# Performance work log

Hardware: AMD Instinct MI355X
Metric: run time of the kernel (lower is better)

## Reference

```python
import jax, jax.numpy as jnp
import numpy as np

N_ITERS = 2
N_NODES = 50000
N_EDGES = 400000
NODE_DIM = 128
EDGE_DIM = 128
MLP_HIDDEN = 128


def _gru_cell(x, h, W_ih, W_hh, b_ih, b_hh):
    # torch.nn.GRUCell math. W_ih: [3H, in], W_hh: [3H, H]
    gi = x @ W_ih.T + b_ih
    gh = h @ W_hh.T + b_hh
    i_r, i_z, i_n = jnp.split(gi, 3, axis=-1)
    h_r, h_z, h_n = jnp.split(gh, 3, axis=-1)
    r = jax.nn.sigmoid(i_r + h_r)
    z = jax.nn.sigmoid(i_z + h_z)
    n = jnp.tanh(i_n + r * h_n)
    return (1.0 - z) * n + z * h


def _edge_softmax(logits, dst, num_nodes):
    # logits: [E], normalized over incoming edges of each dst node
    m = jax.ops.segment_max(logits, dst, num_segments=num_nodes)
    e = jnp.exp(logits - m[dst])
    s = jax.ops.segment_sum(e, dst, num_segments=num_nodes)
    return e / s[dst]


def setup_inputs() -> dict:
    key = jax.random.key(0)
    ks = jax.random.split(key, 20)
    s = 0.05
    inp = {
        'nf': jax.random.normal(ks[0], (N_NODES, NODE_DIM), jnp.float32),
        'ef': jax.random.normal(ks[1], (N_EDGES, EDGE_DIM), jnp.float32),
        'src': jax.random.randint(ks[2], (N_EDGES,), 0, N_NODES, jnp.int32),
        'dst': jax.random.randint(ks[3], (N_EDGES,), 0, N_NODES, jnp.int32),
        # edge GRUCell: input 2*node_dim -> hidden edge_dim
        'eW_ih': s * jax.random.normal(ks[4], (3 * EDGE_DIM, 2 * NODE_DIM), jnp.float32),
        'eW_hh': s * jax.random.normal(ks[5], (3 * EDGE_DIM, EDGE_DIM), jnp.float32),
        'eb_ih': s * jax.random.normal(ks[6], (3 * EDGE_DIM,), jnp.float32),
        'eb_hh': s * jax.random.normal(ks[7], (3 * EDGE_DIM,), jnp.float32),
        # node GRUCell: input edge_dim -> hidden node_dim
        'nW_ih': s * jax.random.normal(ks[8], (3 * NODE_DIM, EDGE_DIM), jnp.float32),
        'nW_hh': s * jax.random.normal(ks[9], (3 * NODE_DIM, NODE_DIM), jnp.float32),
        'nb_ih': s * jax.random.normal(ks[10], (3 * NODE_DIM,), jnp.float32),
        'nb_hh': s * jax.random.normal(ks[11], (3 * NODE_DIM,), jnp.float32),
        # attention MLP: edge_dim -> hidden -> 1
        'aW1': s * jax.random.normal(ks[12], (EDGE_DIM, MLP_HIDDEN), jnp.float32),
        'ab1': jnp.zeros((MLP_HIDDEN,), jnp.float32),
        'aW2': s * jax.random.normal(ks[13], (MLP_HIDDEN, 1), jnp.float32),
        'ab2': jnp.zeros((1,), jnp.float32),
    }
    return inp


def reference(nf, ef, src, dst, eW_ih, eW_hh, eb_ih, eb_hh,
              nW_ih, nW_hh, nb_ih, nb_hh, aW1, ab1, aW2, ab2):
    num_nodes = nf.shape[0]
    for _ in range(N_ITERS):
        # per-edge GRU update: input = [src_h ; dst_h], hidden = edge feature
        x_e = jnp.concatenate([nf[src], nf[dst]], axis=-1)  # [E, 2*node_dim]
        uef = _gru_cell(x_e, ef, eW_ih, eW_hh, eb_ih, eb_hh)  # [E, edge_dim]
        # attention MLP + edge softmax over destination neighborhoods
        logits = (jax.nn.relu(uef @ aW1 + ab1) @ aW2 + ab2)[:, 0]  # [E]
        attn = _edge_softmax(logits, dst, num_nodes)  # [E]
        # weighted scatter-sum aggregation to destination nodes
        agg_m = jax.ops.segment_sum(uef * attn[:, None], dst, num_segments=num_nodes)
        # node GRU update
        unf = _gru_cell(agg_m, nf, nW_ih, nW_hh, nb_ih, nb_hh)  # [N, node_dim]
        nf, ef = unf, uef
    return (nf, ef)
```

## Files before the change

kernel.cpp:

```cpp
#include <hip/hip_runtime.h>

#define NN 50000
#define NE 400000
#define DIM 128

typedef __bf16 bf16x8 __attribute__((ext_vector_type(8)));
typedef float f32x4 __attribute__((ext_vector_type(4)));
typedef unsigned short u16;

#define MFMA16 __builtin_amdgcn_mfma_f32_16x16x32_bf16

__device__ __forceinline__ u16 f2b(float f){ __bf16 b=(__bf16)f; return __builtin_bit_cast(u16,b); }
__device__ __forceinline__ float b2f(u16 h){ unsigned u = ((unsigned)h)<<16; return __builtin_bit_cast(float,u); }
__device__ __forceinline__ float sigm(float x){ return 1.0f/(1.0f+__expf(-x)); }
__device__ __forceinline__ float tanh_(float x){ float e=__expf(2.0f*x); return 1.0f-2.0f/(e+1.0f); }
__device__ __forceinline__ bf16x8 ldb8(const u16* p){ return *reinterpret_cast<const bf16x8*>(p); }

#define GLOAD_LDS(gp, lp) __builtin_amdgcn_global_load_lds( \
    (const __attribute__((address_space(1))) void*)(gp),    \
    (__attribute__((address_space(3))) void*)(lp), 16, 0, 0)

__global__ void f2b_kernel(const float* __restrict__ in, u16* __restrict__ out, int n4){
  int i = blockIdx.x*blockDim.x + threadIdx.x;
  int st = gridDim.x*blockDim.x;
  for (; i<n4; i+=st){
    float4 v = reinterpret_cast<const float4*>(in)[i];
    ushort4 o = { f2b(v.x), f2b(v.y), f2b(v.z), f2b(v.w) };
    reinterpret_cast<ushort4*>(out)[i] = o;
  }
}

__global__ void transpose128_kernel(const float* __restrict__ in, u16* __restrict__ out){
  int i = blockIdx.x*blockDim.x + threadIdx.x;
  int k = i>>7, n = i&127;
  out[n*128+k] = f2b(in[i]);
}

__global__ void zero_kernel(int* p, int n){
  int i = blockIdx.x*blockDim.x + threadIdx.x; if (i<n) p[i]=0;
}
__global__ void hist_kernel(const int* __restrict__ dst, int* __restrict__ counts, int n){
  int i = blockIdx.x*blockDim.x + threadIdx.x; if (i<n) atomicAdd(&counts[dst[i]],1);
}
__global__ void scanA_kernel(const int* __restrict__ counts, int* __restrict__ rowp,
                             int* __restrict__ bsum, int n){
  __shared__ int buf[1024];
  const int gid = blockIdx.x*1024 + threadIdx.x;
  int v = (gid<n) ? counts[gid] : 0;
  buf[threadIdx.x]=v; __syncthreads();
  for (int off=1; off<1024; off<<=1){
    int x = (threadIdx.x>=off) ? buf[threadIdx.x-off] : 0;
    __syncthreads();
    buf[threadIdx.x]+=x; __syncthreads();
  }
  if (gid<n) rowp[gid] = buf[threadIdx.x]-v;
  if (threadIdx.x==1023) bsum[blockIdx.x]=buf[1023];
}
__global__ void scanB_kernel(int* bsum, int* rowp, int nb, int n){
  if (threadIdx.x==0 && blockIdx.x==0){
    int run=0;
    for (int b=0;b<nb;++b){ int t=bsum[b]; bsum[b]=run; run+=t; }
    rowp[n]=run;
  }
}
__global__ void scanC_kernel(int* __restrict__ rowp, int* __restrict__ cursor,
                             const int* __restrict__ bsum, int n){
  const int gid = blockIdx.x*1024 + threadIdx.x;
  if (gid<n){ int v = rowp[gid]+bsum[blockIdx.x]; rowp[gid]=v; cursor[gid]=v; }
}
__global__ void scatter_kernel(const int* __restrict__ dst, int* __restrict__ cursor,
                               int* __restrict__ eids, int n){
  int i = blockIdx.x*blockDim.x + threadIdx.x;
  if (i<n){ int p = atomicAdd(&cursor[dst[i]],1); eids[p]=i; }
}
__global__ void perm_kernel(const int* __restrict__ eids, const int* __restrict__ src,
                            const int* __restrict__ dst, int* __restrict__ srcp,
                            int* __restrict__ dstp, int n){
  int i = blockIdx.x*blockDim.x + threadIdx.x;
  if (i<n){ int e=eids[i]; srcp[i]=src[e]; dstp[i]=dst[e]; }
}
__global__ void efgather_kernel(const int* __restrict__ eids, const float* __restrict__ ef,
                                u16* __restrict__ efb){
  long i = (long)blockIdx.x*256 + threadIdx.x;
  long pos = i>>5; int k4 = (int)(i&31);
  long e = eids[pos];
  float4 v = reinterpret_cast<const float4*>(ef + e*DIM)[k4];
  ushort4 o = { f2b(v.x), f2b(v.y), f2b(v.z), f2b(v.w) };
  reinterpret_cast<ushort4*>(efb + pos*DIM)[k4] = o;
}

__global__ __launch_bounds__(512, 4)
void edge_kernel(const int* __restrict__ srcp, const int* __restrict__ dstp,
                 const int* __restrict__ eids,
                 const u16* __restrict__ nfb, u16* __restrict__ efb,
                 const u16* __restrict__ Wih, const u16* __restrict__ Whh,
                 const float* __restrict__ bih, const float* __restrict__ bhh,
                 const u16* __restrict__ aW1T, const float* __restrict__ ab1,
                 const float* __restrict__ aW2, const float* __restrict__ ab2,
                 float* __restrict__ logits, float* __restrict__ ef32out)
{
  __shared__ __align__(16) u16 wbuf[36*512];
  const int wave = threadIdx.x>>6, lane = threadIdx.x&63;
  const int r16 = lane&15, kq = lane>>4;
  const long base = (long)blockIdx.x*128 + wave*16;
  const long e = base + r16;

  auto stage = [&](int c){
    if (c < 8){
      for (int f = wave; f < 36; f += 8){
        const u16* g;
        if (f < 24){ const int gt = f>>3, s = f&7;
          g = Wih + (long)(gt*128 + c*16 + r16)*256 + s*32 + kq*8; }
        else { const int q = f-24, gt = q>>2, s = q&3;
          g = Whh + (long)(gt*128 + c*16 + r16)*128 + s*32 + kq*8; }
        GLOAD_LDS(g, wbuf + f*512);
      }
    } else {
      for (int f = wave; f < 32; f += 8){
        const int t = f>>2, s = f&3;
        GLOAD_LDS(aW1T + (long)(t*16 + r16)*128 + s*32 + kq*8, wbuf + f*512);
      }
    }
  };

  const u16* sp = nfb + (long)srcp[e]*DIM;
  const u16* dp = nfb + (long)dstp[e]*DIM;
  const u16* ep = efb + e*DIM;
  bf16x8 ag[8], ae[4];
#pragma unroll
  for (int s=0;s<4;++s){
    ag[s]   = ldb8(sp + s*32 + kq*8);
    ag[s+4] = ldb8(dp + s*32 + kq*8);
    ae[s]   = ldb8(ep + s*32 + kq*8);
  }
  int oe[4];
#pragma unroll
  for (int r=0;r<4;++r) oe[r] = eids[base + kq*4 + r];

  stage(0);
  __syncthreads();

  u16* ebase = efb + (base + kq*4)*DIM + r16;
  const float* bi0 = bih + r16;
  const float* bh0 = bhh + r16;

  const f32x4 vzero = {0.f,0.f,0.f,0.f};
  const u16* lbase = wbuf + lane*8;

#pragma unroll 1
  for (int c=0;c<8;++c){
    const int c16 = c*16;
    const float bir=bi0[c16], biz=bi0[c16+DIM], bin=bi0[c16+2*DIM];
    const float bhr=bh0[c16], bhz=bh0[c16+DIM], bhn=bh0[c16+2*DIM];
    float h0p[4];
#pragma unroll
    for (int r=0;r<4;++r) h0p[r] = b2f(ebase[r*DIM + c16]);

    f32x4 ar=vzero, az=vzero, an=vzero, hr=vzero, hz=vzero, hn=vzero;
#pragma unroll
    for (int s=0;s<8;++s){
      ar = MFMA16(ag[s], ldb8(lbase + ( s   )*512), ar,0,0,0);
      az = MFMA16(ag[s], ldb8(lbase + ( 8+s )*512), az,0,0,0);
      an = MFMA16(ag[s], ldb8(lbase + (16+s )*512), an,0,0,0);
    }
#pragma unroll
    for (int s=0;s<4;++s){
      hr = MFMA16(ae[s], ldb8(lbase + (24+s)*512), hr,0,0,0);
      hz = MFMA16(ae[s], ldb8(lbase + (28+s)*512), hz,0,0,0);
      hn = MFMA16(ae[s], ldb8(lbase + (32+s)*512), hn,0,0,0);
    }
    __syncthreads();
    stage(c+1);
    float uv[4];
#pragma unroll
    for (int r=0;r<4;++r){
      float rg = sigm(ar[r]+bir + hr[r]+bhr);
      float zg = sigm(az[r]+biz + hz[r]+bhz);
      float ng = tanh_(an[r]+bin + rg*(hn[r]+bhn));
      float u  = ng + zg*(h0p[r]-ng);
      ebase[r*DIM + c16] = f2b(u);
      uv[r] = u;
    }
    if (ef32out){
#pragma unroll
      for (int r=0;r<4;++r) ef32out[(long)oe[r]*DIM + c16 + r16] = uv[r];
    }
    __syncthreads();
  }

  bf16x8 ua[4];
#pragma unroll
  for (int s=0;s<4;++s) ua[s] = ldb8(ep + s*32 + kq*8);
  float part[4] = {0.f,0.f,0.f,0.f};
#pragma unroll 1
  for (int t=0;t<8;++t){
    f32x4 h = vzero;
#pragma unroll
    for (int s=0;s<4;++s)
      h = MFMA16(ua[s], ldb8(lbase + (t*4+s)*512), h,0,0,0);
    const int cc = t*16 + r16;
    const float b1 = ab1[cc], w2 = aW2[cc];
#pragma unroll
    for (int r=0;r<4;++r) part[r] += fmaxf(h[r]+b1, 0.f)*w2;
  }
#pragma unroll
  for (int off=1; off<16; off<<=1){
#pragma unroll
    for (int r=0;r<4;++r) part[r] += __shfl_xor(part[r], off, 64);
  }
  if (r16==0){
    const float b2v = ab2[0];
#pragma unroll
    for (int r=0;r<4;++r) logits[base + kq*4 + r] = part[r] + b2v;
  }
}

__global__ __launch_bounds__(256)
void agg_kernel(const int* __restrict__ rowp, const float* __restrict__ logits,
                const u16* __restrict__ uefb, u16* __restrict__ aggb)
{
  const int wave = threadIdx.x>>6, lane = threadIdx.x&63;
  const int v = blockIdx.x*4 + wave;
  if (v>=NN) return;
  const int p0 = rowp[v], p1 = rowp[v+1], deg = p1-p0;
  float ax=0.f, ay=0.f;
  if (deg>0){
    float mx = -__builtin_inff();
    for (int i=p0+lane; i<p1; i+=64) mx = fmaxf(mx, logits[i]);
#pragma unroll
    for (int off=32; off; off>>=1) mx = fmaxf(mx, __shfl_xor(mx, off, 64));
    float ss = 0.f;
    for (int i=p0+lane; i<p1; i+=64) ss += __expf(logits[i] - mx);
#pragma unroll
    for (int off=32; off; off>>=1) ss += __shfl_xor(ss, off, 64);
    const float inv = 1.0f/ss;
    int i = p0;
    for (; i+2<=p1; i+=2){
      const float l0 = logits[i], l1 = logits[i+1];
      const unsigned q0 = *reinterpret_cast<const unsigned*>(uefb + (long)i*DIM + lane*2);
      const unsigned q1 = *reinterpret_cast<const unsigned*>(uefb + (long)(i+1)*DIM + lane*2);
      const float a0 = __expf(l0-mx)*inv, a1 = __expf(l1-mx)*inv;
      ax += a0*b2f((u16)q0) + a1*b2f((u16)q1);
      ay += a0*b2f((u16)(q0>>16)) + a1*b2f((u16)(q1>>16));
    }
    if (i<p1){
      const float a0 = __expf(logits[i]-mx)*inv;
      const unsigned q0 = *reinterpret_cast<const unsigned*>(uefb + (long)i*DIM + lane*2);
      ax += a0*b2f((u16)q0);
      ay += a0*b2f((u16)(q0>>16));
    }
  }
  unsigned pack = (unsigned)f2b(ax) | ((unsigned)f2b(ay)<<16);
  *reinterpret_cast<unsigned*>(aggb + (long)v*DIM + lane*2) = pack;
}

__global__ __launch_bounds__(512, 4)
void node_kernel(const u16* __restrict__ aggb, u16* __restrict__ nfb,
                 const float* nf32, float* unf32,
                 const u16* __restrict__ Wih, const u16* __restrict__ Whh,
                 const float* __restrict__ bih, const float* __restrict__ bhh)
{
  __shared__ __align__(16) u16 wbuf[2*24*512];
  const int wave = threadIdx.x>>6, lane = threadIdx.x&63;
  const int r16 = lane&15, kq = lane>>4;
  const long tbase = (long)blockIdx.x*128 + wave*16;
  const long v = tbase + r16;
  const long vcl = (v < NN) ? v : (NN-1);

  auto stage = [&](int c){
    if (c >= 8) return;
    u16* bufp = wbuf + (c&1)*24*512;
    for (int f = wave; f < 24; f += 8){
      const u16* g;
      if (f < 12){ const int gt = f>>2, s = f&3;
        g = Wih + (long)(gt*128 + c*16 + r16)*128 + s*32 + kq*8; }
      else { const int q = f-12, gt = q>>2, s = q&3;
        g = Whh + (long)(gt*128 + c*16 + r16)*128 + s*32 + kq*8; }
      GLOAD_LDS(g, bufp + f*512);
    }
  };

  bf16x8 xa[4], ha[4];
#pragma unroll
  for (int s=0;s<4;++s){
    xa[s] = ldb8(aggb + vcl*DIM + s*32 + kq*8);
    ha[s] = ldb8(nfb  + vcl*DIM + s*32 + kq*8);
  }
  stage(0);
  __syncthreads();

  const f32x4 vzero = {0.f,0.f,0.f,0.f};

#pragma unroll 1
  for (int c=0;c<8;++c){
    stage(c+1);
    const int oc = c*16 + r16;
    const float bir=bih[oc], biz=bih[DIM+oc], bin=bih[2*DIM+oc];
    const float bhr=bhh[oc], bhz=bhh[DIM+oc], bhn=bhh[2*DIM+oc];
    float h0p[4];
#pragma unroll
    for (int r=0;r<4;++r){
      const long rr = tbase + kq*4 + r;
      h0p[r] = (rr < NN) ? nf32[rr*DIM+oc] : 0.f;
    }
    const u16* lb = wbuf + (c&1)*24*512 + lane*8;
    f32x4 ar=vzero, az=vzero, an=vzero, hr=vzero, hz=vzero, hn=vzero;
#pragma unroll
    for (int s=0;s<4;++s){
      ar=MFMA16(xa[s], ldb8(lb + ( s   )*512), ar,0,0,0);
      az=MFMA16(xa[s], ldb8(lb + ( 4+s)*512), az,0,0,0);
      an=MFMA16(xa[s], ldb8(lb + ( 8+s)*512), an,0,0,0);
      hr=MFMA16(ha[s], ldb8(lb + (12+s)*512), hr,0,0,0);
      hz=MFMA16(ha[s], ldb8(lb + (16+s)*512), hz,0,0,0);
      hn=MFMA16(ha[s], ldb8(lb + (20+s)*512), hn,0,0,0);
    }
#pragma unroll
    for (int r=0;r<4;++r){
      const long rr = tbase + kq*4 + r;
      if (rr < NN){
        float rg = sigm(ar[r]+bir + hr[r]+bhr);
        float zg = sigm(az[r]+biz + hz[r]+bhz);
        float ng = tanh_(an[r]+bin + rg*(hn[r]+bhn));
        float u  = ng + zg*(h0p[r]-ng);
        unf32[rr*DIM+oc] = u;
        nfb[rr*DIM+oc] = f2b(u);
      }
    }
    __syncthreads();
  }
}

extern "C" void kernel_launch(void* const* d_in, const int* in_sizes, int n_in,
                              void* d_out, int out_size, void* d_ws, size_t ws_size,
                              hipStream_t stream)
{
  const float* nf_in = (const float*)d_in[0];
  const float* ef_in = (const float*)d_in[1];
  const int*   src   = (const int*)d_in[2];
  const int*   dst   = (const int*)d_in[3];
  const float* eWih  = (const float*)d_in[4];
  const float* eWhh  = (const float*)d_in[5];
  const float* ebih  = (const float*)d_in[6];
  const float* ebhh  = (const float*)d_in[7];
  const float* nWih  = (const float*)d_in[8];
  const float* nWhh  = (const float*)d_in[9];
  const float* nbih  = (const float*)d_in[10];
  const float* nbhh  = (const float*)d_in[11];
  const float* aW1   = (const float*)d_in[12];
  const float* ab1   = (const float*)d_in[13];
  const float* aW2   = (const float*)d_in[14];
  const float* ab2   = (const float*)d_in[15];

  float* nf_out = (float*)d_out;
  float* ef_out = nf_out + (size_t)NN*DIM;

  char* p = (char*)d_ws;
  auto carve = [&](size_t bytes)->void*{ void* r = (void*)p; p += (bytes + 255) & ~(size_t)255; return r; };
  u16* efb    = (u16*)carve((size_t)NE*DIM*2);
  u16* nfb    = (u16*)carve((size_t)NN*DIM*2);
  u16* aggb   = (u16*)carve((size_t)NN*DIM*2);
  float* logits = (float*)carve((size_t)NE*4);
  int* eids   = (int*)carve((size_t)NE*4);
  int* srcp   = (int*)carve((size_t)NE*4);
  int* dstp   = (int*)carve((size_t)NE*4);
  int* counts = (int*)carve((size_t)NN*4);
  int* rowp   = (int*)carve((size_t)(NN+1)*4);
  int* cursor = (int*)carve((size_t)NN*4);
  int* bsum   = (int*)carve((size_t)64*4);
  u16* bWih   = (u16*)carve((size_t)384*256*2);
  u16* bWhh   = (u16*)carve((size_t)384*128*2);
  u16* bnWih  = (u16*)carve((size_t)384*128*2);
  u16* bnWhh  = (u16*)carve((size_t)384*128*2);
  u16* baW1T  = (u16*)carve((size_t)128*128*2);

  const int NB = (NN + 1023)/1024;

  zero_kernel<<<(NN+255)/256,256,0,stream>>>(counts, NN);
  hist_kernel<<<(NE+255)/256,256,0,stream>>>(dst, counts, NE);
  scanA_kernel<<<NB,1024,0,stream>>>(counts, rowp, bsum, NN);
  scanB_kernel<<<1,64,0,stream>>>(bsum, rowp, NB, NN);
  scanC_kernel<<<NB,1024,0,stream>>>(rowp, cursor, bsum, NN);
  scatter_kernel<<<(NE+255)/256,256,0,stream>>>(dst, cursor, eids, NE);
  perm_kernel<<<(NE+255)/256,256,0,stream>>>(eids, src, dst, srcp, dstp, NE);

  f2b_kernel<<<2048,256,0,stream>>>(nf_in, nfb, NN*DIM/4);
  efgather_kernel<<<NE*32/256,256,0,stream>>>(eids, ef_in, efb);
  f2b_kernel<<<96,256,0,stream>>>(eWih, bWih, 384*256/4);
  f2b_kernel<<<48,256,0,stream>>>(eWhh, bWhh, 384*128/4);
  f2b_kernel<<<48,256,0,stream>>>(nWih, bnWih, 384*128/4);
  f2b_kernel<<<48,256,0,stream>>>(nWhh, bnWhh, 384*128/4);
  transpose128_kernel<<<64,256,0,stream>>>(aW1, baW1T);

  for (int it=0; it<2; ++it){
    const float* nf_cur = (it==0) ? nf_in : nf_out;
    float* efout32 = (it==1) ? ef_out : nullptr;
    edge_kernel<<<NE/128,512,0,stream>>>(srcp, dstp, eids, nfb, efb,
                                         bWih, bWhh, ebih, ebhh,
                                         baW1T, ab1, aW2, ab2, logits, efout32);
    agg_kernel<<<(NN+3)/4,256,0,stream>>>(rowp, logits, efb, aggb);
    node_kernel<<<(NN+127)/128,512,0,stream>>>(aggb, nfb, nf_cur, nf_out,
                                               bnWih, bnWhh, nbih, nbhh);
  }
}
```

Before: 800.6 us.

## Process two output column tiles per edge-GRU stage and fuse weight prep launches

The edge kernel now stages weights for two 16-column chunks per iteration, doubling the LDS buffer to 72 tiles. This halves the number of barrier/stage rounds from 8 to 4 and uses precomputed, incrementally advanced global pointers. It also folds the ih/hh accumulators for the r and z gates together, so the combined bias is added once. Five weight-conversion launches are merged into one kernel and a zero kernel is replaced with hipMemsetAsync. The larger LDS footprint may reduce occupancy under the 512x4 launch bounds.

Result: slower. 1.194 ms (+49.1%).

```diff
diff --git a/kernel.cpp b/kernel.cpp
--- a/kernel.cpp
+++ b/kernel.cpp
@@ -30,15 +30,24 @@
   }
 }
 
-__global__ void transpose128_kernel(const float* __restrict__ in, u16* __restrict__ out){
-  int i = blockIdx.x*blockDim.x + threadIdx.x;
-  int k = i>>7, n = i&127;
-  out[n*128+k] = f2b(in[i]);
-}
-
-__global__ void zero_kernel(int* p, int n){
-  int i = blockIdx.x*blockDim.x + threadIdx.x; if (i<n) p[i]=0;
-}
+__global__ void wprep_kernel(const float* __restrict__ eWih, const float* __restrict__ eWhh,
+                             const float* __restrict__ nWih, const float* __restrict__ nWhh,
+                             const float* __restrict__ aW1,
+                             u16* __restrict__ bWih, u16* __restrict__ bWhh,
+                             u16* __restrict__ bnWih, u16* __restrict__ bnWhh,
+                             u16* __restrict__ baW1T){
+  int i = blockIdx.x*256 + threadIdx.x;
+  if (i < 98304){ bWih[i] = f2b(eWih[i]); return; }
+  i -= 98304;
+  if (i < 49152){ bWhh[i] = f2b(eWhh[i]); return; }
+  i -= 49152;
+  if (i < 49152){ bnWih[i] = f2b(nWih[i]); return; }
+  i -= 49152;
+  if (i < 49152){ bnWhh[i] = f2b(nWhh[i]); return; }
+  i -= 49152;
+  { int k = i>>7, n = i&127; baW1T[n*128+k] = f2b(aW1[i]); }
+}
+
 __global__ void hist_kernel(const int* __restrict__ dst, int* __restrict__ counts, int n){
   int i = blockIdx.x*blockDim.x + threadIdx.x; if (i<n) atomicAdd(&counts[dst[i]],1);
 }
@@ -99,27 +108,42 @@
                  const float* __restrict__ aW2, const float* __restrict__ ab2,
                  float* __restrict__ logits, float* __restrict__ ef32out)
 {
-  __shared__ __align__(16) u16 wbuf[36*512];
+  __shared__ __align__(16) u16 wbuf[72*512];
   const int wave = threadIdx.x>>6, lane = threadIdx.x&63;
   const int r16 = lane&15, kq = lane>>4;
   const long base = (long)blockIdx.x*128 + wave*16;
   const long e = base + r16;
 
-  auto stage = [&](int c){
-    if (c < 8){
-      for (int f = wave; f < 36; f += 8){
-        const u16* g;
-        if (f < 24){ const int gt = f>>3, s = f&7;
-          g = Wih + (long)(gt*128 + c*16 + r16)*256 + s*32 + kq*8; }
-        else { const int q = f-24, gt = q>>2, s = q&3;
-          g = Whh + (long)(gt*128 + c*16 + r16)*128 + s*32 + kq*8; }
-        GLOAD_LDS(g, wbuf + f*512);
-      }
+  const u16* pk[9];
+  int adv[9];
+#pragma unroll
+  for (int k=0;k<9;++k){
+    const int f = wave + k*8;
+    const int h = (f>=36) ? 1 : 0;
+    const int ff = f - h*36;
+    if (ff < 24){
+      const int gt = ff>>3, s = ff&7;
+      pk[k] = Wih + (long)(gt*128 + h*16 + r16)*256 + s*32 + kq*8;
+      adv[k] = 32*256;
     } else {
-      for (int f = wave; f < 32; f += 8){
-        const int t = f>>2, s = f&3;
-        GLOAD_LDS(aW1T + (long)(t*16 + r16)*128 + s*32 + kq*8, wbuf + f*512);
-      }
+      const int q = ff-24, gt = q>>2, s = q&3;
+      pk[k] = Whh + (long)(gt*128 + h*16 + r16)*128 + s*32 + kq*8;
+      adv[k] = 32*128;
+    }
+  }
+  auto stageC = [&](){
+#pragma unroll
+    for (int k=0;k<9;++k){
+      GLOAD_LDS(pk[k], wbuf + (wave + k*8)*512);
+      pk[k] += adv[k];
+    }
+  };
+  auto stageAttn = [&](){
+#pragma unroll
+    for (int k=0;k<4;++k){
+      const int f = wave + k*8;
+      const int t = f>>2, s = f&3;
+      GLOAD_LDS(aW1T + (long)(t*16 + r16)*128 + s*32 + kq*8, wbuf + f*512);
     }
   };
 
@@ -137,7 +161,7 @@
 #pragma unroll
   for (int r=0;r<4;++r) oe[r] = eids[base + kq*4 + r];
 
-  stage(0);
+  stageC();
   __syncthreads();
 
   u16* ebase = efb + (base + kq*4)*DIM + r16;
@@ -148,42 +172,56 @@
   const u16* lbase = wbuf + lane*8;
 
 #pragma unroll 1
-  for (int c=0;c<8;++c){
-    const int c16 = c*16;
-    const float bir=bi0[c16], biz=bi0[c16+DIM], bin=bi0[c16+2*DIM];
-    const float bhr=bh0[c16], bhz=bh0[c16+DIM], bhn=bh0[c16+2*DIM];
-    float h0p[4];
-#pragma unroll
-    for (int r=0;r<4;++r) h0p[r] = b2f(ebase[r*DIM + c16]);
-
-    f32x4 ar=vzero, az=vzero, an=vzero, hr=vzero, hz=vzero, hn=vzero;
-#pragma unroll
-    for (int s=0;s<8;++s){
-      ar = MFMA16(ag[s], ldb8(lbase + ( s   )*512), ar,0,0,0);
-      az = MFMA16(ag[s], ldb8(lbase + ( 8+s )*512), az,0,0,0);
-      an = MFMA16(ag[s], ldb8(lbase + (16+s )*512), an,0,0,0);
-    }
-#pragma unroll
-    for (int s=0;s<4;++s){
-      hr = MFMA16(ae[s], ldb8(lbase + (24+s)*512), hr,0,0,0);
-      hz = MFMA16(ae[s], ldb8(lbase + (28+s)*512), hz,0,0,0);
-      hn = MFMA16(ae[s], ldb8(lbase + (32+s)*512), hn,0,0,0);
+  for (int C=0;C<4;++C){
+    const int c32 = C*32;
+    float h0p[2][4];
+#pragma unroll
+    for (int h2=0;h2<2;++h2)
+#pragma unroll
+      for (int r=0;r<4;++r) h0p[h2][r] = b2f(ebase[r*DIM + c32 + h2*16]);
+
+    f32x4 aR[2],aZ[2],aNi[2],aNh[2];
+#pragma unroll
+    for (int h2=0;h2<2;++h2){ aR[h2]=vzero; aZ[h2]=vzero; aNi[h2]=vzero; aNh[h2]=vzero; }
+#pragma unroll
+    for (int h2=0;h2<2;++h2){
+      const u16* lb = lbase + h2*36*512;
+#pragma unroll
+      for (int s=0;s<8;++s){
+        aR[h2]  = MFMA16(ag[s], ldb8(lb + ( s   )*512), aR[h2] ,0,0,0);
+        aZ[h2]  = MFMA16(ag[s], ldb8(lb + ( 8+s )*512), aZ[h2] ,0,0,0);
+        aNi[h2] = MFMA16(ag[s], ldb8(lb + (16+s )*512), aNi[h2],0,0,0);
+      }
+#pragma unroll
+      for (int s=0;s<4;++s){
+        aR[h2]  = MFMA16(ae[s], ldb8(lb + (24+s)*512), aR[h2] ,0,0,0);
+        aZ[h2]  = MFMA16(ae[s], ldb8(lb + (28+s)*512), aZ[h2] ,0,0,0);
+        aNh[h2] = MFMA16(ae[s], ldb8(lb + (32+s)*512), aNh[h2],0,0,0);
+      }
     }
     __syncthreads();
-    stage(c+1);
-    float uv[4];
-#pragma unroll
-    for (int r=0;r<4;++r){
-      float rg = sigm(ar[r]+bir + hr[r]+bhr);
-      float zg = sigm(az[r]+biz + hz[r]+bhz);
-      float ng = tanh_(an[r]+bin + rg*(hn[r]+bhn));
-      float u  = ng + zg*(h0p[r]-ng);
-      ebase[r*DIM + c16] = f2b(u);
-      uv[r] = u;
-    }
-    if (ef32out){
-#pragma unroll
-      for (int r=0;r<4;++r) ef32out[(long)oe[r]*DIM + c16 + r16] = uv[r];
+    if (C < 3) stageC(); else stageAttn();
+#pragma unroll
+    for (int h2=0;h2<2;++h2){
+      const int c16 = c32 + h2*16;
+      const float btR = bi0[c16]       + bh0[c16];
+      const float btZ = bi0[c16+DIM]   + bh0[c16+DIM];
+      const float bin = bi0[c16+2*DIM];
+      const float bhn = bh0[c16+2*DIM];
+      float uv[4];
+#pragma unroll
+      for (int r=0;r<4;++r){
+        float rg = sigm(aR[h2][r] + btR);
+        float zg = sigm(aZ[h2][r] + btZ);
+        float ng = tanh_(aNi[h2][r] + bin + rg*(aNh[h2][r] + bhn));
+        float u  = ng + zg*(h0p[h2][r]-ng);
+        ebase[r*DIM + c16] = f2b(u);
+        uv[r] = u;
+      }
+      if (ef32out){
+#pragma unroll
+        for (int r=0;r<4;++r) ef32out[(long)oe[r]*DIM + c16 + r16] = uv[r];
+      }
     }
     __syncthreads();
   }
@@ -375,7 +413,7 @@
 
   const int NB = (NN + 1023)/1024;
 
-  zero_kernel<<<(NN+255)/256,256,0,stream>>>(counts, NN);
+  hipMemsetAsync(counts, 0, (size_t)NN*4, stream);
   hist_kernel<<<(NE+255)/256,256,0,stream>>>(dst, counts, NE);
   scanA_kernel<<<NB,1024,0,stream>>>(counts, rowp, bsum, NN);
   scanB_kernel<<<1,64,0,stream>>>(bsum, rowp, NB, NN);
@@ -385,11 +423,8 @@
 
   f2b_kernel<<<2048,256,0,stream>>>(nf_in, nfb, NN*DIM/4);
   efgather_kernel<<<NE*32/256,256,0,stream>>>(eids, ef_in, efb);
-  f2b_kernel<<<96,256,0,stream>>>(eWih, bWih, 384*256/4);
-  f2b_kernel<<<48,256,0,stream>>>(eWhh, bWhh, 384*128/4);
-  f2b_kernel<<<48,256,0,stream>>>(nWih, bnWih, 384*128/4);
-  f2b_kernel<<<48,256,0,stream>>>(nWhh, bnWhh, 384*128/4);
-  transpose128_kernel<<<64,256,0,stream>>>(aW1, baW1T);
+  wprep_kernel<<<1024,256,0,stream>>>(eWih, eWhh, nWih, nWhh, aW1,
+                                      bWih, bWhh, bnWih, bnWhh, baW1T);
 
   for (int it=0; it<2; ++it){
     const float* nf_cur = (it==0) ? nf_in : nf_out;
```

## Halve edge kernel block size and merge weight-conversion launches

Applied to the files above, without the earlier changes.

The edge kernel now runs 256-thread blocks covering 64 edges instead of 512 threads covering 128, and its weight staging loops step by 4 waves. Each block has fewer waves sharing one LDS weight tile, so more blocks can fit per CU and there is less barrier contention. The cost is that each weight chunk gets staged into LDS by twice as many blocks. The five weight-conversion launches are merged into one kernel, and the zeroing kernel is replaced by hipMemsetAsync to cut launch overhead.

Result: slower. 960.8 us (+20.0%).

```diff
diff --git a/kernel.cpp b/kernel.cpp
--- a/kernel.cpp
+++ b/kernel.cpp
@@ -30,15 +30,24 @@
   }
 }
 
-__global__ void transpose128_kernel(const float* __restrict__ in, u16* __restrict__ out){
-  int i = blockIdx.x*blockDim.x + threadIdx.x;
-  int k = i>>7, n = i&127;
-  out[n*128+k] = f2b(in[i]);
-}
-
-__global__ void zero_kernel(int* p, int n){
-  int i = blockIdx.x*blockDim.x + threadIdx.x; if (i<n) p[i]=0;
-}
+__global__ void wprep_kernel(const float* __restrict__ eWih, const float* __restrict__ eWhh,
+                             const float* __restrict__ nWih, const float* __restrict__ nWhh,
+                             const float* __restrict__ aW1,
+                             u16* __restrict__ bWih, u16* __restrict__ bWhh,
+                             u16* __restrict__ bnWih, u16* __restrict__ bnWhh,
+                             u16* __restrict__ baW1T){
+  int i = blockIdx.x*256 + threadIdx.x;
+  if (i < 98304){ bWih[i] = f2b(eWih[i]); return; }
+  i -= 98304;
+  if (i < 49152){ bWhh[i] = f2b(eWhh[i]); return; }
+  i -= 49152;
+  if (i < 49152){ bnWih[i] = f2b(nWih[i]); return; }
+  i -= 49152;
+  if (i < 49152){ bnWhh[i] = f2b(nWhh[i]); return; }
+  i -= 49152;
+  { int k = i>>7, n = i&127; baW1T[n*128+k] = f2b(aW1[i]); }
+}
+
 __global__ void hist_kernel(const int* __restrict__ dst, int* __restrict__ counts, int n){
   int i = blockIdx.x*blockDim.x + threadIdx.x; if (i<n) atomicAdd(&counts[dst[i]],1);
 }
@@ -89,7 +98,7 @@
   reinterpret_cast<ushort4*>(efb + pos*DIM)[k4] = o;
 }
 
-__global__ __launch_bounds__(512, 4)
+__global__ __launch_bounds__(256, 4)
 void edge_kernel(const int* __restrict__ srcp, const int* __restrict__ dstp,
                  const int* __restrict__ eids,
                  const u16* __restrict__ nfb, u16* __restrict__ efb,
@@ -102,12 +111,12 @@
   __shared__ __align__(16) u16 wbuf[36*512];
   const int wave = threadIdx.x>>6, lane = threadIdx.x&63;
   const int r16 = lane&15, kq = lane>>4;
-  const long base = (long)blockIdx.x*128 + wave*16;
+  const long base = (long)blockIdx.x*64 + wave*16;
   const long e = base + r16;
 
   auto stage = [&](int c){
     if (c < 8){
-      for (int f = wave; f < 36; f += 8){
+      for (int f = wave; f < 36; f += 4){
         const u16* g;
         if (f < 24){ const int gt = f>>3, s = f&7;
           g = Wih + (long)(gt*128 + c*16 + r16)*256 + s*32 + kq*8; }
@@ -116,7 +125,7 @@
         GLOAD_LDS(g, wbuf + f*512);
       }
     } else {
-      for (int f = wave; f < 32; f += 8){
+      for (int f = wave; f < 32; f += 4){
         const int t = f>>2, s = f&3;
         GLOAD_LDS(aW1T + (long)(t*16 + r16)*128 + s*32 + kq*8, wbuf + f*512);
       }
@@ -375,7 +384,7 @@
 
   const int NB = (NN + 1023)/1024;
 
-  zero_kernel<<<(NN+255)/256,256,0,stream>>>(counts, NN);
+  hipMemsetAsync(counts, 0, (size_t)NN*4, stream);
   hist_kernel<<<(NE+255)/256,256,0,stream>>>(dst, counts, NE);
   scanA_kernel<<<NB,1024,0,stream>>>(counts, rowp, bsum, NN);
   scanB_kernel<<<1,64,0,stream>>>(bsum, rowp, NB, NN);
@@ -385,18 +394,15 @@
 
   f2b_kernel<<<2048,256,0,stream>>>(nf_in, nfb, NN*DIM/4);
   efgather_kernel<<<NE*32/256,256,0,stream>>>(eids, ef_in, efb);
-  f2b_kernel<<<96,256,0,stream>>>(eWih, bWih, 384*256/4);
-  f2b_kernel<<<48,256,0,stream>>>(eWhh, bWhh, 384*128/4);
-  f2b_kernel<<<48,256,0,stream>>>(nWih, bnWih, 384*128/4);
-  f2b_kernel<<<48,256,0,stream>>>(nWhh, bnWhh, 384*128/4);
-  transpose128_kernel<<<64,256,0,stream>>>(aW1, baW1T);
+  wprep_kernel<<<1024,256,0,stream>>>(eWih, eWhh, nWih, nWhh, aW1,
+                                      bWih, bWhh, bnWih, bnWhh, baW1T);
 
   for (int it=0; it<2; ++it){
     const float* nf_cur = (it==0) ? nf_in : nf_out;
     float* efout32 = (it==1) ? ef_out : nullptr;
-    edge_kernel<<<NE/128,512,0,stream>>>(srcp, dstp, eids, nfb, efb,
-                                         bWih, bWhh, ebih, ebhh,
-                                         baW1T, ab1, aW2, ab2, logits, efout32);
+    edge_kernel<<<NE/64,256,0,stream>>>(srcp, dstp, eids, nfb, efb,
+                                        bWih, bWhh, ebih, ebhh,
+                                        baW1T, ab1, aW2, ab2, logits, efout32);
     agg_kernel<<<(NN+3)/4,256,0,stream>>>(rowp, logits, efb, aggb);
     node_kernel<<<(NN+127)/128,512,0,stream>>>(aggb, nfb, nf_cur, nf_out,
                                                bnWih, bnWhh, nbih, nbhh);
```
